# Kernel tuning notes

Measured on AMD Instinct MI355X. Metric: run time of the kernel, lower is better.

## Reference

```python
import jax, jax.numpy as jnp
import numpy as np

B, D = 16384, 2048


def setup_inputs() -> dict:
    key = jax.random.key(0)
    k1, k2, k3 = jax.random.split(key, 3)
    stdv = 1.0 / np.sqrt(D)
    initial = jax.random.normal(k1, (B, D), dtype=jnp.float32)
    X = jax.random.normal(k2, (B, D), dtype=jnp.float32)
    alphas = jax.random.uniform(k3, (D, 1), dtype=jnp.float32, minval=-stdv, maxval=stdv)
    bias = jnp.zeros((D,), dtype=jnp.float32)
    return {"initial": initial, "X": X, "alphas": alphas, "bias": bias}


def reference(initial, X, alphas, bias):
    # Original: bmm(initial[:,:,None], X[:,None,:]) @ alphas -> squeeze, + bias + X.
    # bmm outer product followed by reduction against alphas is exactly
    # initial * (X @ alphas), avoiding the (B, d, d) intermediate.
    scale = X @ alphas            # (B, 1) == X \cdot alphas per row
    return initial * scale + X + bias  # broadcast bias (d,) over batch
```

## Files before the change

### kernel.cpp

```cpp
#include <hip/hip_runtime.h>


#define CN_D 2048
#define CN_ROWS 16384

typedef float vfloat4 __attribute__((ext_vector_type(4)));

__global__ __attribute__((amdgpu_waves_per_eu(4, 8)))
__launch_bounds__(256) void crossnet_kernel(
    const float* __restrict__ initial,
    const float* __restrict__ X,
    const float* __restrict__ alphas,
    const float* __restrict__ bias,
    float* __restrict__ out)
{
    const int wave = threadIdx.x >> 6;
    const int lane = threadIdx.x & 63;
    const int row  = (blockIdx.x << 2) + wave;

    const vfloat4* __restrict__ Xrow = (const vfloat4*)(X       + (size_t)row * CN_D);
    const vfloat4* __restrict__ Irow = (const vfloat4*)(initial + (size_t)row * CN_D);
    const vfloat4* __restrict__ A4   = (const vfloat4*)alphas;
    const vfloat4* __restrict__ B4   = (const vfloat4*)bias;
    vfloat4*       __restrict__ Orow = (vfloat4*)(out + (size_t)row * CN_D);

    vfloat4 x[8];
    vfloat4 fi[8];

#pragma unroll
    for (int k = 0; k < 8; ++k) x[k]  = Xrow[(k << 6) + lane];
#pragma unroll
    for (int k = 0; k < 8; ++k) fi[k] = Irow[(k << 6) + lane];

    float acc = 0.0f;
#pragma unroll
    for (int k = 0; k < 8; ++k) {
        const vfloat4 a = A4[(k << 6) + lane];
        acc += x[k].x * a.x + x[k].y * a.y + x[k].z * a.z + x[k].w * a.w;
    }

#pragma unroll
    for (int k = 0; k < 8; ++k) {
        const vfloat4 b = B4[(k << 6) + lane];
        x[k] += b;
    }

#pragma unroll
    for (int k = 0; k < 8; ++k) {
        asm volatile("" : "+v"(x[k]));
        asm volatile("" : "+v"(fi[k]));
    }

#pragma unroll
    for (int off = 32; off > 0; off >>= 1)
        acc += __shfl_xor(acc, off, 64);

#pragma unroll
    for (int k = 0; k < 8; ++k) {
        vfloat4 o;
        o.x = fmaf(fi[k].x, acc, x[k].x);
        o.y = fmaf(fi[k].y, acc, x[k].y);
        o.z = fmaf(fi[k].z, acc, x[k].z);
        o.w = fmaf(fi[k].w, acc, x[k].w);
        __builtin_nontemporal_store(o, &Orow[(k << 6) + lane]);
    }
}

extern "C" void kernel_launch(void* const* d_in, const int* in_sizes, int n_in,
                              void* d_out, int out_size, void* d_ws, size_t ws_size,
                              hipStream_t stream) {
    const float* initial = (const float*)d_in[0];
    const float* X       = (const float*)d_in[1];
    const float* alphas  = (const float*)d_in[2];
    const float* bias    = (const float*)d_in[3];
    float* out = (float*)d_out;

    crossnet_kernel<<<CN_ROWS / 4, 256, 0, stream>>>(initial, X, alphas, bias, out);
}
```

Baseline: 319.8 us.

## Use persistent waves with LDS-cached alphas/bias and prefetch next row's X

```diff
diff --git a/kernel.cpp b/kernel.cpp
--- a/kernel.cpp
+++ b/kernel.cpp
@@ -3,66 +3,95 @@
 
 #define CN_D 2048
 #define CN_ROWS 16384
+#define CN_BLOCKS 1024
+#define CN_WAVES (CN_BLOCKS * 4)
+#define CN_ROWS_PER_WAVE (CN_ROWS / CN_WAVES)
 
 typedef float vfloat4 __attribute__((ext_vector_type(4)));
 
-__global__ __attribute__((amdgpu_waves_per_eu(4, 8)))
-__launch_bounds__(256) void crossnet_kernel(
+__global__ __launch_bounds__(256, 4) void crossnet_kernel(
     const float* __restrict__ initial,
     const float* __restrict__ X,
     const float* __restrict__ alphas,
     const float* __restrict__ bias,
     float* __restrict__ out)
 {
+    __shared__ float lds_a[CN_D];
+    __shared__ float lds_b[CN_D];
+
     const int wave = threadIdx.x >> 6;
     const int lane = threadIdx.x & 63;
-    const int row  = (blockIdx.x << 2) + wave;
+    const int r0   = (blockIdx.x << 2) + wave;
 
-    const vfloat4* __restrict__ Xrow = (const vfloat4*)(X       + (size_t)row * CN_D);
-    const vfloat4* __restrict__ Irow = (const vfloat4*)(initial + (size_t)row * CN_D);
-    const vfloat4* __restrict__ A4   = (const vfloat4*)alphas;
-    const vfloat4* __restrict__ B4   = (const vfloat4*)bias;
-    vfloat4*       __restrict__ Orow = (vfloat4*)(out + (size_t)row * CN_D);
+    vfloat4 xc[8];
+    {
+        const vfloat4* Xr = (const vfloat4*)(X + (size_t)r0 * CN_D);
+#pragma unroll
+        for (int k = 0; k < 8; ++k) xc[k] = Xr[(k << 6) + lane];
+    }
 
-    vfloat4 x[8];
-    vfloat4 fi[8];
+    {
+        const vfloat4* A4 = (const vfloat4*)alphas;
+        const vfloat4* B4 = (const vfloat4*)bias;
+        vfloat4* LA = (vfloat4*)lds_a;
+        vfloat4* LB = (vfloat4*)lds_b;
+        const int t = threadIdx.x;
+        LA[t]       = A4[t];
+        LA[t + 256] = A4[t + 256];
+        LB[t]       = B4[t];
+        LB[t + 256] = B4[t + 256];
+    }
+    __syncthreads();
+
+    const vfloat4* LA = (const vfloat4*)lds_a;
+    const vfloat4* LB = (const vfloat4*)lds_b;
 
 #pragma unroll
-    for (int k = 0; k < 8; ++k) x[k]  = Xrow[(k << 6) + lane];
+    for (int it = 0; it < CN_ROWS_PER_WAVE; ++it) {
+        const int r = r0 + (it << 12);
+        const vfloat4* Ir = (const vfloat4*)(initial + (size_t)r * CN_D);
+        vfloat4*       Or = (vfloat4*)(out     + (size_t)r * CN_D);
+
+        vfloat4 fi[8];
 #pragma unroll
-    for (int k = 0; k < 8; ++k) fi[k] = Irow[(k << 6) + lane];
+        for (int k = 0; k < 8; ++k) fi[k] = Ir[(k << 6) + lane];
 
-    float acc = 0.0f;
+        vfloat4 xn[8];
+        if (it + 1 < CN_ROWS_PER_WAVE) {
+            const vfloat4* Xn = (const vfloat4*)(X + (size_t)(r + 4096) * CN_D);
 #pragma unroll
-    for (int k = 0; k < 8; ++k) {
-        const vfloat4 a = A4[(k << 6) + lane];
-        acc += x[k].x * a.x + x[k].y * a.y + x[k].z * a.z + x[k].w * a.w;
-    }
+            for (int k = 0; k < 8; ++k) xn[k] = Xn[(k << 6) + lane];
+        }
+
+        float acc = 0.0f;
+#pragma unroll
+        for (int k = 0; k < 8; ++k) {
+            const vfloat4 a = LA[(k << 6) + lane];
+            acc = fmaf(xc[k].x, a.x, acc);
+            acc = fmaf(xc[k].y, a.y, acc);
+            acc = fmaf(xc[k].z, a.z, acc);
+            acc = fmaf(xc[k].w, a.w, acc);
+        }
 
 #pragma unroll
-    for (int k = 0; k < 8; ++k) {
-        const vfloat4 b = B4[(k << 6) + lane];
-        x[k] += b;
-    }
+        for (int off = 32; off > 0; off >>= 1)
+            acc += __shfl_xor(acc, off, 64);
 
 #pragma unroll
-    for (int k = 0; k < 8; ++k) {
-        asm volatile("" : "+v"(x[k]));
-        asm volatile("" : "+v"(fi[k]));
-    }
+        for (int k = 0; k < 8; ++k) {
+            const vfloat4 b = LB[(k << 6) + lane];
+            vfloat4 o;
+            o.x = fmaf(fi[k].x, acc, xc[k].x + b.x);
+            o.y = fmaf(fi[k].y, acc, xc[k].y + b.y);
+            o.z = fmaf(fi[k].z, acc, xc[k].z + b.z);
+            o.w = fmaf(fi[k].w, acc, xc[k].w + b.w);
+            Or[(k << 6) + lane] = o;
+        }
 
+        if (it + 1 < CN_ROWS_PER_WAVE) {
 #pragma unroll
-    for (int off = 32; off > 0; off >>= 1)
-        acc += __shfl_xor(acc, off, 64);
-
-#pragma unroll
-    for (int k = 0; k < 8; ++k) {
-        vfloat4 o;
-        o.x = fmaf(fi[k].x, acc, x[k].x);
-        o.y = fmaf(fi[k].y, acc, x[k].y);
-        o.z = fmaf(fi[k].z, acc, x[k].z);
-        o.w = fmaf(fi[k].w, acc, x[k].w);
-        __builtin_nontemporal_store(o, &Orow[(k << 6) + lane]);
+            for (int k = 0; k < 8; ++k) xc[k] = xn[k];
+        }
     }
 }
 
@@ -75,5 +104,5 @@
     const float* bias    = (const float*)d_in[3];
     float* out = (float*)d_out;
 
-    crossnet_kernel<<<CN_ROWS / 4, 256, 0, stream>>>(initial, X, alphas, bias, out);
+    crossnet_kernel<<<CN_BLOCKS, 256, 0, stream>>>(initial, X, alphas, bias, out);
 }
```

After: 312.5 us. -2.3%, faster.
